# Performance work log

Hardware: AMD Instinct MI355X
Metric: run time of the kernel (lower is better)

The kernel has to match this reference:

```python
import jax, jax.numpy as jnp
import numpy as np

N = 500_000      # total observations
D = 40           # per-observation feature dim
S = 2048         # number of segments (time series)
WIDTH = 128      # psi hidden width
LATENT = 128     # latent width
DOT = 64         # dot_prod_dim
HEADS = 4        # n_heads


def setup_inputs() -> dict:
    key = jax.random.key(0)
    ks = jax.random.split(key, 12)

    def he(k, shape):
        fan_in = shape[0]
        lim = np.sqrt(6.0 / fan_in)
        return jax.random.uniform(k, shape, jnp.float32, -lim, lim)

    inputs = jax.random.normal(ks[0], (N, D), jnp.float32)
    segment_ids = jnp.sort(jax.random.randint(ks[1], (N,), 0, S))
    lengths = jax.random.randint(ks[2], (S,), 0, 300)
    return {
        "inputs": inputs,
        "segment_ids": segment_ids,
        "lengths": lengths,
        "W1": he(ks[3], (D, WIDTH)),      "b1": jnp.zeros((WIDTH,), jnp.float32),
        "W2": he(ks[4], (WIDTH, WIDTH)), "b2": jnp.zeros((WIDTH,), jnp.float32),
        "W3": he(ks[5], (WIDTH, LATENT)),"b3": jnp.zeros((LATENT,), jnp.float32),
        "Wr": he(ks[6], (LATENT, LATENT)),"br": jnp.zeros((LATENT,), jnp.float32),
        "W_k": he(ks[7], (LATENT + D, DOT * HEADS)),
        "W_q": jax.random.normal(ks[8], (HEADS, DOT), jnp.float32) * 0.02,
    }


def segment_softmax(x, seg, num_segments):
    # x: [N, H]; softmax over elements sharing the same segment id
    m = jax.ops.segment_max(x, seg, num_segments, indices_are_sorted=True)
    e = jnp.exp(x - m[seg])
    denom = jax.ops.segment_sum(e, seg, num_segments, indices_are_sorted=True)
    return e / denom[seg]


def reference(inputs, segment_ids, lengths, W1, b1, W2, b2, W3, b3, Wr, br, W_k, W_q):
    relu = jax.nn.relu
    # psi: 2 hidden dense layers + latent projection (all relu)
    h = relu(inputs @ W1 + b1)
    h = relu(h @ W2 + b2)
    enc = relu(h @ W3 + b3)                                   # [N, LATENT]
    # segment mean aggregation
    sums = jax.ops.segment_sum(enc, segment_ids, S, indices_are_sorted=True)
    counts = jax.ops.segment_sum(jnp.ones((enc.shape[0], 1), enc.dtype),
                                 segment_ids, S, indices_are_sorted=True)
    agg = sums / jnp.maximum(counts, 1.0)                      # [S, LATENT]
    agg = relu(agg @ Wr + br)                                  # rho
    # broadcast back and combine
    combined = jnp.concatenate([inputs, agg[segment_ids]], axis=-1)  # [N, D+LATENT]
    keys = (combined @ W_k).reshape(-1, HEADS, DOT)            # split+stack == reshape
    preattn = jnp.einsum('nhd,hd->nh', keys, W_q) / jnp.sqrt(jnp.float32(DOT))
    attn = segment_softmax(preattn, segment_ids, S)            # [N, H]
    # match original: list of per-head [N, 1] tensors -> stacked [H, N, 1]
    return jnp.transpose(attn)[..., None]
```

## Files before the change

kernel.cpp:

```cpp
#include <hip/hip_runtime.h>
#include <math.h>


#define NROWS 500000
#define DIM 40
#define NQ (DIM / 4)
#define NSEG 2048
#define DOTD 64
#define NH 4
#define PBLOCK 256
#define CROWS 512

__global__ __launch_bounds__(PBLOCK) void prep_kernel(
    const int* __restrict__ seg,
    const float* __restrict__ Wk,
    const float* __restrict__ Wq,
    int* __restrict__ seg_start,
    int* __restrict__ seg_end,
    float* __restrict__ wxg)
{
    const int tid = (int)threadIdx.x;
    const int n = (int)(blockIdx.x * PBLOCK + tid);

    if (blockIdx.x == 0 && tid < DIM * NH) {
        const int h = tid / DIM;
        const int d = tid - h * DIM;
        const float* wkp = Wk + d * (NH * DOTD) + h * DOTD;
        const float* wqp = Wq + h * DOTD;
        float acc = 0.f;
        #pragma unroll
        for (int j = 0; j < DOTD; ++j) acc += wkp[j] * wqp[j];
        wxg[h * DIM + d] = acc * 0.125f;
    }

    if (n < NROWS) {
        const int s = seg[n];
        if (n == 0) {
            seg_start[s] = 0;
            for (int t = 0; t < s; ++t) { seg_start[t] = 0; seg_end[t] = 0; }
        } else {
            const int sp = seg[n - 1];
            if (sp != s) {
                seg_start[s] = n;
                seg_end[sp] = n;
                for (int t = sp + 1; t < s; ++t) { seg_start[t] = n; seg_end[t] = n; }
            }
        }
        if (n == NROWS - 1) {
            seg_end[s] = NROWS;
            for (int t = s + 1; t < NSEG; ++t) { seg_start[t] = NROWS; seg_end[t] = NROWS; }
        }
    }
}

__global__ __launch_bounds__(PBLOCK) void logits_kernel(
    const float* __restrict__ x,
    const float* __restrict__ wxg,
    float* __restrict__ logit)
{
    __shared__ __align__(16) float wxl[NH][DIM];

    const int tid = (int)threadIdx.x;
    {
        float* wf = &wxl[0][0];
        for (int t = tid; t < NH * DIM; t += PBLOCK) wf[t] = wxg[t];
    }
    __syncthreads();

    const int n = (int)(blockIdx.x * PBLOCK + tid);
    if (n >= NROWS) return;

    const float4* xr = (const float4*)(x + (size_t)n * DIM);
    float a[NH] = {0.f, 0.f, 0.f, 0.f};
    #pragma unroll
    for (int q = 0; q < NQ; ++q) {
        const float4 v = xr[q];
        #pragma unroll
        for (int h = 0; h < NH; ++h) {
            const float4 w = ((const float4*)wxl[h])[q];
            a[h] += v.x * w.x + v.y * w.y + v.z * w.z + v.w * w.w;
        }
    }
    #pragma unroll
    for (int h = 0; h < NH; ++h)
        logit[(size_t)h * NROWS + n] = a[h];
}

__global__ __launch_bounds__(64) void seg_softmax_kernel(
    const float* __restrict__ logit,
    const int* __restrict__ seg_start,
    const int* __restrict__ seg_end,
    float* __restrict__ out)
{
    __shared__ float cache[NH][CROWS];

    const int lane = (int)threadIdx.x;
    const int s = (int)blockIdx.x;
    const int start = seg_start[s];
    const int rows = seg_end[s] - start;
    if (rows <= 0) return;

    float lmax[NH];
    #pragma unroll
    for (int h = 0; h < NH; ++h) lmax[h] = -3.0e38f;

    for (int i = lane; i < rows; i += 64) {
        #pragma unroll
        for (int h = 0; h < NH; ++h) {
            const float v = logit[(size_t)h * NROWS + start + i];
            if (i < CROWS) cache[h][i] = v;
            lmax[h] = fmaxf(lmax[h], v);
        }
    }

    float m[NH];
    #pragma unroll
    for (int h = 0; h < NH; ++h) {
        float v = lmax[h];
        #pragma unroll
        for (int off = 32; off > 0; off >>= 1) v = fmaxf(v, __shfl_xor(v, off, 64));
        m[h] = v;
    }

    float lsum[NH] = {0.f, 0.f, 0.f, 0.f};
    for (int i = lane; i < rows; i += 64) {
        #pragma unroll
        for (int h = 0; h < NH; ++h) {
            const float l = (i < CROWS) ? cache[h][i]
                                        : logit[(size_t)h * NROWS + start + i];
            const float e = __expf(l - m[h]);
            if (i < CROWS) cache[h][i] = e;
            lsum[h] += e;
        }
    }
    float rden[NH];
    #pragma unroll
    for (int h = 0; h < NH; ++h) {
        float v = lsum[h];
        #pragma unroll
        for (int off = 32; off > 0; off >>= 1) v += __shfl_xor(v, off, 64);
        rden[h] = 1.0f / v;
    }

    for (int i = lane; i < rows; i += 64) {
        const int n = start + i;
        #pragma unroll
        for (int h = 0; h < NH; ++h) {
            const float e = (i < CROWS)
                ? cache[h][i]
                : __expf(logit[(size_t)h * NROWS + n] - m[h]);
            out[(size_t)h * NROWS + n] = e * rden[h];
        }
    }
}

extern "C" void kernel_launch(void* const* d_in, const int* in_sizes, int n_in,
                              void* d_out, int out_size, void* d_ws, size_t ws_size,
                              hipStream_t stream) {
    const float* x  = (const float*)d_in[0];
    const int* seg  = (const int*)d_in[1];
    const float* Wk = (const float*)d_in[11];
    const float* Wq = (const float*)d_in[12];
    float* out = (float*)d_out;

    int* seg_start = (int*)d_ws;
    int* seg_end   = seg_start + NSEG;
    float* wxg     = (float*)(seg_end + NSEG);
    float* logit   = wxg + 256;

    const int nblk = (NROWS + PBLOCK - 1) / PBLOCK;
    hipLaunchKernelGGL(prep_kernel, dim3(nblk), dim3(PBLOCK),
                       0, stream, seg, Wk, Wq, seg_start, seg_end, wxg);
    hipLaunchKernelGGL(logits_kernel, dim3(nblk), dim3(PBLOCK),
                       0, stream, x, wxg, logit);
    hipLaunchKernelGGL(seg_softmax_kernel, dim3(NSEG), dim3(64),
                       0, stream, logit, seg_start, seg_end, out);
}
```

Before: 157.8 us.

## Fuse prep into logits kernel, interleave logits, use online softmax

Merges the segment-boundary and weight-folding prep kernel into the logits kernel. Every block now recomputes the folded Wk·Wq vector into shared memory, which removes one launch and the global round trip for the folded weights. Logits are stored interleaved as float4 per row so the softmax kernel can read all heads in one vector load. The softmax switches to a single-pass online max/sum with exponentials recomputed in the output pass, dropping a pass over the data. The cost is redundant weight folding in every block and more exp calls per element.

```diff
diff --git a/kernel.cpp b/kernel.cpp
--- a/kernel.cpp
+++ b/kernel.cpp
@@ -8,67 +8,57 @@
 #define NSEG 2048
 #define DOTD 64
 #define NH 4
-#define PBLOCK 256
+#define ABLOCK 256
 #define CROWS 512
 
-__global__ __launch_bounds__(PBLOCK) void prep_kernel(
+__global__ __launch_bounds__(ABLOCK) void fused_logits_kernel(
+    const float* __restrict__ x,
     const int* __restrict__ seg,
     const float* __restrict__ Wk,
     const float* __restrict__ Wq,
     int* __restrict__ seg_start,
     int* __restrict__ seg_end,
-    float* __restrict__ wxg)
-{
-    const int tid = (int)threadIdx.x;
-    const int n = (int)(blockIdx.x * PBLOCK + tid);
-
-    if (blockIdx.x == 0 && tid < DIM * NH) {
-        const int h = tid / DIM;
-        const int d = tid - h * DIM;
-        const float* wkp = Wk + d * (NH * DOTD) + h * DOTD;
-        const float* wqp = Wq + h * DOTD;
-        float acc = 0.f;
-        #pragma unroll
-        for (int j = 0; j < DOTD; ++j) acc += wkp[j] * wqp[j];
-        wxg[h * DIM + d] = acc * 0.125f;
-    }
-
-    if (n < NROWS) {
-        const int s = seg[n];
-        if (n == 0) {
-            seg_start[s] = 0;
-            for (int t = 0; t < s; ++t) { seg_start[t] = 0; seg_end[t] = 0; }
-        } else {
-            const int sp = seg[n - 1];
-            if (sp != s) {
-                seg_start[s] = n;
-                seg_end[sp] = n;
-                for (int t = sp + 1; t < s; ++t) { seg_start[t] = n; seg_end[t] = n; }
-            }
-        }
-        if (n == NROWS - 1) {
-            seg_end[s] = NROWS;
-            for (int t = s + 1; t < NSEG; ++t) { seg_start[t] = NROWS; seg_end[t] = NROWS; }
-        }
-    }
-}
-
-__global__ __launch_bounds__(PBLOCK) void logits_kernel(
-    const float* __restrict__ x,
-    const float* __restrict__ wxg,
-    float* __restrict__ logit)
+    float4* __restrict__ logit4)
 {
     __shared__ __align__(16) float wxl[NH][DIM];
 
     const int tid = (int)threadIdx.x;
-    {
-        float* wf = &wxl[0][0];
-        for (int t = tid; t < NH * DIM; t += PBLOCK) wf[t] = wxg[t];
+
+    if (tid < DIM * NH) {
+        const int h = tid & 3;
+        const int d = tid >> 2;
+        const float4* wkp = (const float4*)(Wk + d * (NH * DOTD) + h * DOTD);
+        const float4* wqp = (const float4*)(Wq + h * DOTD);
+        float acc = 0.f;
+        #pragma unroll
+        for (int j = 0; j < DOTD / 4; ++j) {
+            const float4 a = wkp[j];
+            const float4 b = wqp[j];
+            acc += a.x * b.x + a.y * b.y + a.z * b.z + a.w * b.w;
+        }
+        wxl[h][d] = acc * 0.125f;
     }
     __syncthreads();
 
-    const int n = (int)(blockIdx.x * PBLOCK + tid);
+    const int n = (int)(blockIdx.x * ABLOCK + tid);
     if (n >= NROWS) return;
+
+    const int s = seg[n];
+    if (n == 0) {
+        seg_start[s] = 0;
+        for (int t = 0; t < s; ++t) { seg_start[t] = 0; seg_end[t] = 0; }
+    } else {
+        const int sp = seg[n - 1];
+        if (sp != s) {
+            seg_start[s] = n;
+            seg_end[sp] = n;
+            for (int t = sp + 1; t < s; ++t) { seg_start[t] = n; seg_end[t] = n; }
+        }
+    }
+    if (n == NROWS - 1) {
+        seg_end[s] = NROWS;
+        for (int t = s + 1; t < NSEG; ++t) { seg_start[t] = NROWS; seg_end[t] = NROWS; }
+    }
 
     const float4* xr = (const float4*)(x + (size_t)n * DIM);
     float a[NH] = {0.f, 0.f, 0.f, 0.f};
@@ -81,18 +71,16 @@
             a[h] += v.x * w.x + v.y * w.y + v.z * w.z + v.w * w.w;
         }
     }
-    #pragma unroll
-    for (int h = 0; h < NH; ++h)
-        logit[(size_t)h * NROWS + n] = a[h];
+    logit4[n] = make_float4(a[0], a[1], a[2], a[3]);
 }
 
 __global__ __launch_bounds__(64) void seg_softmax_kernel(
-    const float* __restrict__ logit,
+    const float4* __restrict__ logit4,
     const int* __restrict__ seg_start,
     const int* __restrict__ seg_end,
     float* __restrict__ out)
 {
-    __shared__ float cache[NH][CROWS];
+    __shared__ __align__(16) float4 cache4[CROWS];
 
     const int lane = (int)threadIdx.x;
     const int s = (int)blockIdx.x;
@@ -100,57 +88,42 @@
     const int rows = seg_end[s] - start;
     if (rows <= 0) return;
 
-    float lmax[NH];
+    float ml[NH], sl[NH];
     #pragma unroll
-    for (int h = 0; h < NH; ++h) lmax[h] = -3.0e38f;
+    for (int h = 0; h < NH; ++h) { ml[h] = -3.0e38f; sl[h] = 0.f; }
 
     for (int i = lane; i < rows; i += 64) {
+        const float4 l4 = logit4[start + i];
+        if (i < CROWS) cache4[i] = l4;
+        const float l[NH] = {l4.x, l4.y, l4.z, l4.w};
         #pragma unroll
         for (int h = 0; h < NH; ++h) {
-            const float v = logit[(size_t)h * NROWS + start + i];
-            if (i < CROWS) cache[h][i] = v;
-            lmax[h] = fmaxf(lmax[h], v);
+            const float nm = fmaxf(ml[h], l[h]);
+            sl[h] = sl[h] * __expf(ml[h] - nm) + __expf(l[h] - nm);
+            ml[h] = nm;
         }
     }
 
-    float m[NH];
+    float m[NH], rden[NH];
     #pragma unroll
     for (int h = 0; h < NH; ++h) {
-        float v = lmax[h];
+        float M = ml[h];
         #pragma unroll
-        for (int off = 32; off > 0; off >>= 1) v = fmaxf(v, __shfl_xor(v, off, 64));
-        m[h] = v;
-    }
-
-    float lsum[NH] = {0.f, 0.f, 0.f, 0.f};
-    for (int i = lane; i < rows; i += 64) {
+        for (int off = 32; off > 0; off >>= 1) M = fmaxf(M, __shfl_xor(M, off, 64));
+        float S = sl[h] * __expf(ml[h] - M);
         #pragma unroll
-        for (int h = 0; h < NH; ++h) {
-            const float l = (i < CROWS) ? cache[h][i]
-                                        : logit[(size_t)h * NROWS + start + i];
-            const float e = __expf(l - m[h]);
-            if (i < CROWS) cache[h][i] = e;
-            lsum[h] += e;
-        }
-    }
-    float rden[NH];
-    #pragma unroll
-    for (int h = 0; h < NH; ++h) {
-        float v = lsum[h];
-        #pragma unroll
-        for (int off = 32; off > 0; off >>= 1) v += __shfl_xor(v, off, 64);
-        rden[h] = 1.0f / v;
+        for (int off = 32; off > 0; off >>= 1) S += __shfl_xor(S, off, 64);
+        m[h] = M;
+        rden[h] = 1.0f / S;
     }
 
     for (int i = lane; i < rows; i += 64) {
+        const float4 l4 = (i < CROWS) ? cache4[i] : logit4[start + i];
+        const float l[NH] = {l4.x, l4.y, l4.z, l4.w};
         const int n = start + i;
         #pragma unroll
-        for (int h = 0; h < NH; ++h) {
-            const float e = (i < CROWS)
-                ? cache[h][i]
-                : __expf(logit[(size_t)h * NROWS + n] - m[h]);
-            out[(size_t)h * NROWS + n] = e * rden[h];
-        }
+        for (int h = 0; h < NH; ++h)
+            out[(size_t)h * NROWS + n] = __expf(l[h] - m[h]) * rden[h];
     }
 }
 
@@ -165,14 +138,11 @@
 
     int* seg_start = (int*)d_ws;
     int* seg_end   = seg_start + NSEG;
-    float* wxg     = (float*)(seg_end + NSEG);
-    float* logit   = wxg + 256;
+    float4* logit4 = (float4*)((char*)d_ws + 16384);
 
-    const int nblk = (NROWS + PBLOCK - 1) / PBLOCK;
-    hipLaunchKernelGGL(prep_kernel, dim3(nblk), dim3(PBLOCK),
-                       0, stream, seg, Wk, Wq, seg_start, seg_end, wxg);
-    hipLaunchKernelGGL(logits_kernel, dim3(nblk), dim3(PBLOCK),
-                       0, stream, x, wxg, logit);
+    const int nblk = (NROWS + ABLOCK - 1) / ABLOCK;
+    hipLaunchKernelGGL(fused_logits_kernel, dim3(nblk), dim3(ABLOCK),
+                       0, stream, x, seg, Wk, Wq, seg_start, seg_end, logit4);
     hipLaunchKernelGGL(seg_softmax_kernel, dim3(NSEG), dim3(64),
-                       0, stream, logit, seg_start, seg_end, out);
+                       0, stream, logit4, seg_start, seg_end, out);
 }
```

After: 163.1 us. +3.3%, slower.
